# Kernel tuning notes

Measured on AMD Instinct MI355X. Metric: run time of the kernel, lower is better.

The kernel has to match this reference:

```python
import jax, jax.numpy as jnp
import numpy as np

N_NODES = 100000
N_EDGES = 1200000
NODE_IN = 64
EDGE_IN = 32
HIDDEN = 64


def _glorot(key, shape):
    fan_in, fan_out = shape[0], shape[1]
    s = jnp.sqrt(2.0 / (fan_in + fan_out))
    return jax.random.normal(key, shape, dtype=jnp.float32) * s


def setup_inputs() -> dict:
    key = jax.random.key(0)
    ks = jax.random.split(key, 16)
    inp = {
        "x": jax.random.normal(ks[0], (N_NODES, NODE_IN), dtype=jnp.float32),
        "edge_index": jax.random.randint(ks[1], (2, N_EDGES), 0, N_NODES, dtype=jnp.int64),
        "edge_attr": jax.random.normal(ks[2], (N_EDGES, EDGE_IN), dtype=jnp.float32),
        # SAGE layer 0 (in=NODE_IN -> HIDDEN): lin_l (neighbors, has bias), lin_r (root)
        "w_l0": _glorot(ks[3], (NODE_IN, HIDDEN)),
        "w_r0": _glorot(ks[4], (NODE_IN, HIDDEN)),
        "b0": jnp.zeros((HIDDEN,), jnp.float32),
        "ln_g0": jnp.ones((HIDDEN,), jnp.float32),
        "ln_b0": jnp.zeros((HIDDEN,), jnp.float32),
        # SAGE layer 1 (HIDDEN -> HIDDEN)
        "w_l1": _glorot(ks[5], (HIDDEN, HIDDEN)),
        "w_r1": _glorot(ks[6], (HIDDEN, HIDDEN)),
        "b1": jnp.zeros((HIDDEN,), jnp.float32),
        "ln_g1": jnp.ones((HIDDEN,), jnp.float32),
        "ln_b1": jnp.zeros((HIDDEN,), jnp.float32),
        # Edge classifier MLP: in_dim = 3*HIDDEN + EDGE_IN = 224
        "cw1": _glorot(ks[7], (3 * HIDDEN + EDGE_IN, HIDDEN)),
        "cb1": jnp.zeros((HIDDEN,), jnp.float32),
        "cw2": _glorot(ks[8], (HIDDEN, HIDDEN // 2)),
        "cb2": jnp.zeros((HIDDEN // 2,), jnp.float32),
        "cw3": _glorot(ks[9], (HIDDEN // 2, 1)),
        "cb3": jnp.zeros((1,), jnp.float32),
    }
    return inp


def _sage_conv(x, src, dst, w_l, w_r, b):
    # mean-aggregate source features at destination nodes (PyG SAGEConv, aggr='mean')
    n = x.shape[0]
    msg = x[src]  # [E, F] gather
    agg = jax.ops.segment_sum(msg, dst, num_segments=n)
    cnt = jax.ops.segment_sum(jnp.ones((src.shape[0], 1), x.dtype), dst, num_segments=n)
    mean = agg / jnp.maximum(cnt, 1.0)
    return mean @ w_l + x @ w_r + b


def _layer_norm(x, g, b, eps=1e-5):
    mu = jnp.mean(x, axis=-1, keepdims=True)
    var = jnp.var(x, axis=-1, keepdims=True)
    return (x - mu) * jax.lax.rsqrt(var + eps) * g + b


def reference(x, edge_index, edge_attr,
              w_l0, w_r0, b0, ln_g0, ln_b0,
              w_l1, w_r1, b1, ln_g1, ln_b1,
              cw1, cb1, cw2, cb2, cw3, cb3):
    src, dst = edge_index[0], edge_index[1]
    # Encoder (eval mode: dropout is identity)
    h = jax.nn.relu(_layer_norm(_sage_conv(x, src, dst, w_l0, w_r0, b0), ln_g0, ln_b0))
    z = jax.nn.relu(_layer_norm(_sage_conv(h, src, dst, w_l1, w_r1, b1), ln_g1, ln_b1))
    # Edge classifier: gather-concat-MLP
    z_src = z[src]
    z_dst = z[dst]
    edge_repr = jnp.concatenate([z_src, z_dst, z_src * z_dst, edge_attr], axis=-1)
    h1 = jax.nn.relu(edge_repr @ cw1 + cb1)
    h2 = jax.nn.relu(h1 @ cw2 + cb2)
    logits = (h2 @ cw3 + cb3).squeeze(-1)  # [E]
    return logits
```

## Files before the change

### kernel.cpp

```cpp
#include <hip/hip_runtime.h>
#include <hip/hip_bf16.h>

#define N_NODES 100000
#define N_EDGES 1200000

typedef __attribute__((ext_vector_type(8))) short bfrag;
typedef __attribute__((ext_vector_type(4))) float ffrag;

union FragU { uint4 v; uint32_t u[4]; bfrag f; };

__device__ __forceinline__ ushort bfbits(float a) {
  union { __hip_bfloat16 h; ushort u; } c; c.h = __float2bfloat16(a); return c.u;
}
__device__ __forceinline__ uint32_t pkbf(float a, float b) {
  union { __hip_bfloat162 h; uint32_t u; } c;
  c.h = __float22bfloat162_rn(float2{a, b}); return c.u;
}
__device__ __forceinline__ uint32_t mul2bf(uint32_t a, uint32_t b) {
  union { uint32_t u; __hip_bfloat162 h; } x, y, r;
  x.u = a; y.u = b; r.h = __hmul2(x.h, y.h); return r.u;
}
__device__ __forceinline__ float bflo(uint32_t u) { return __int_as_float(u << 16); }
__device__ __forceinline__ float bfhi(uint32_t u) { return __int_as_float(u & 0xffff0000u); }


__global__ void cvt_k(const float* __restrict__ x, ushort* __restrict__ xb, int n2) {
  int i = blockIdx.x * blockDim.x + threadIdx.x;
  if (i < n2) {
    float2 v = ((const float2*)x)[i];
    ((uint32_t*)xb)[i] = pkbf(v.x, v.y);
  }
}


__global__ void hist_k(const int* __restrict__ ei, int* __restrict__ deg,
                       int* __restrict__ rank, int E) {
  int e = blockIdx.x * blockDim.x + threadIdx.x;
  if (e < E) rank[e] = atomicAdd(&deg[ei[E + e]], 1);
}

__global__ __launch_bounds__(1024) void scan1_k(const int* __restrict__ deg,
                                                int* __restrict__ off,
                                                int* __restrict__ bsum, int n) {
  __shared__ int wpart[16];
  __shared__ int wpre[16];
  int tid = threadIdx.x, lane = tid & 63, wid = tid >> 6;
  int i = blockIdx.x * 1024 + tid;
  int v = (i < n) ? deg[i] : 0;
  int x = v;
  #pragma unroll
  for (int o = 1; o < 64; o <<= 1) {
    int y = __shfl_up(x, o);
    if (lane >= o) x += y;
  }
  if (lane == 63) wpart[wid] = x;
  __syncthreads();
  if (tid == 0) {
    int run = 0;
    #pragma unroll
    for (int w = 0; w < 16; w++) { int t = wpart[w]; wpre[w] = run; run += t; }
    bsum[blockIdx.x] = run;
  }
  __syncthreads();
  if (i < n) off[i] = x - v + wpre[wid];
}

__global__ void scan2_k(const int* __restrict__ bsum, int* __restrict__ bpre,
                        int* __restrict__ off, int nb, int n) {
  if (threadIdx.x == 0) {
    int run = 0;
    for (int b = 0; b < nb; b++) { int t = bsum[b]; bpre[b] = run; run += t; }
    off[n] = run;
  }
}

__global__ __launch_bounds__(1024) void scan3_k(int* __restrict__ off,
                                                const int* __restrict__ bpre, int n) {
  int i = blockIdx.x * 1024 + threadIdx.x;
  if (i < n) off[i] += bpre[blockIdx.x];
}

__global__ void fill_k(const int* __restrict__ ei, const int* __restrict__ off,
                       const int* __restrict__ rank, int* __restrict__ csr, int E) {
  int e = blockIdx.x * blockDim.x + threadIdx.x;
  if (e < E) {
    int d = ei[E + e];
    int p = off[d] + rank[e];
    __builtin_nontemporal_store(ei[e], &csr[p]);
  }
}


__global__ __launch_bounds__(256) void agg_k(
    const ushort* __restrict__ Xb, const int* __restrict__ off, const int* __restrict__ csr,
    ushort* __restrict__ aggout, int n) {
  int lane = threadIdx.x & 63;
  int quad = lane >> 4, f8 = lane & 15;
  int wave = blockIdx.x * 4 + (threadIdx.x >> 6);
  int nw = gridDim.x * 4;
  int nquads = (n + 3) >> 2;
  const uint2* X2 = (const uint2*)Xb;
  for (int p = wave; p < nquads; p += nw) {
    int i = p * 4 + quad;
    int ic = i < n ? i : n - 1;
    int s0 = off[ic], s1 = off[ic + 1];
    float a0 = 0.f, a1 = 0.f, a2 = 0.f, a3 = 0.f;
    for (int j = s0; j < s1; j += 8) {
      int id[8]; uint2 us[8];
      #pragma unroll
      for (int u = 0; u < 8; u++) {
        int jj = j + u;
        id[u] = csr[jj < s1 ? jj : s1 - 1];
      }
      #pragma unroll
      for (int u = 0; u < 8; u++) us[u] = X2[(size_t)id[u] * 16 + f8];
      #pragma unroll
      for (int u = 0; u < 8; u++) {
        if (j + u < s1) {
          a0 += bflo(us[u].x); a1 += bfhi(us[u].x);
          a2 += bflo(us[u].y); a3 += bfhi(us[u].y);
        }
      }
    }
    if (i < n) {
      float rdeg = 1.f / fmaxf((float)(s1 - s0), 1.f);
      uint2 w;
      w.x = pkbf(a0 * rdeg, a1 * rdeg);
      w.y = pkbf(a2 * rdeg, a3 * rdeg);
      ((uint2*)aggout)[(size_t)i * 16 + f8] = w;
    }
  }
}


__global__ __launch_bounds__(256) void node_k(
    const ushort* __restrict__ agg, const ushort* __restrict__ selfb,
    const float* __restrict__ wl, const float* __restrict__ wr,
    const float* __restrict__ bias, const float* __restrict__ g, const float* __restrict__ lb,
    ushort* __restrict__ outb, int n) {
  __shared__ ushort wt[64 * 128];
  const int tid = threadIdx.x;
  for (int i = tid; i < 8192; i += 256) {
    int k = i >> 6, nn = i & 63;
    float v = (k < 64) ? wl[k * 64 + nn] : wr[(k - 64) * 64 + nn];
    wt[nn * 128 + (((k >> 3) ^ (nn & 7)) * 8) + (k & 7)] = bfbits(v);
  }
  __syncthreads();
  const int lane = tid & 63, wid = tid >> 6;
  const int ln = lane & 15, q = lane >> 4;
  float bias_n[4], g_n[4], lb_n[4];
  #pragma unroll
  for (int nt = 0; nt < 4; nt++) {
    bias_n[nt] = bias[nt * 16 + ln];
    g_n[nt] = g[nt * 16 + ln];
    lb_n[nt] = lb[nt * 16 + ln];
  }
  const int ntiles = (n + 15) >> 4;
  for (int t = blockIdx.x * 4 + wid; t < ntiles; t += gridDim.x * 4) {
    int node = t * 16 + ln;
    int nc = node < n ? node : n - 1;
    FragU afr[4];
    #pragma unroll
    for (int kk = 0; kk < 2; kk++) {
      afr[kk].v     = ((const uint4*)agg)[(size_t)nc * 8 + kk * 4 + q];
      afr[2 + kk].v = ((const uint4*)selfb)[(size_t)nc * 8 + kk * 4 + q];
    }
    ffrag acc[4];
    #pragma unroll
    for (int nt = 0; nt < 4; nt++) acc[nt] = ffrag{0.f, 0.f, 0.f, 0.f};
    #pragma unroll
    for (int kk = 0; kk < 4; kk++) {
      bfrag a = afr[kk].f;
      #pragma unroll
      for (int nt = 0; nt < 4; nt++) {
        int nn = nt * 16 + ln;
        int b = kk * 4 + q;
        const bfrag* bp = (const bfrag*)&wt[nn * 128 + ((b ^ (nn & 7)) * 8)];
        acc[nt] = __builtin_amdgcn_mfma_f32_16x16x32_bf16(a, *bp, acc[nt], 0, 0, 0);
      }
    }
    #pragma unroll
    for (int r = 0; r < 4; r++) {
      int m = t * 16 + q * 4 + r;
      float o[4];
      #pragma unroll
      for (int nt = 0; nt < 4; nt++) o[nt] = acc[nt][r] + bias_n[nt];
      float s = (o[0] + o[1]) + (o[2] + o[3]);
      #pragma unroll
      for (int mm = 1; mm < 16; mm <<= 1) s += __shfl_xor(s, mm);
      float mu = s * (1.f / 64.f);
      float v2 = 0.f;
      #pragma unroll
      for (int nt = 0; nt < 4; nt++) { float d2 = o[nt] - mu; v2 += d2 * d2; }
      #pragma unroll
      for (int mm = 1; mm < 16; mm <<= 1) v2 += __shfl_xor(v2, mm);
      float rs = rsqrtf(v2 * (1.f / 64.f) + 1e-5f);
      if (m < n) {
        #pragma unroll
        for (int nt = 0; nt < 4; nt++) {
          float y = fmaxf((o[nt] - mu) * rs * g_n[nt] + lb_n[nt], 0.f);
          outb[(size_t)m * 64 + nt * 16 + ln] = bfbits(y);
        }
      }
    }
  }
}


__global__ __launch_bounds__(256) void edge_mfma_k(
    const int* __restrict__ ei, const float* __restrict__ ea,
    const ushort* __restrict__ zb,
    const float* __restrict__ cw1, const float* __restrict__ cb1,
    const float* __restrict__ cw2, const float* __restrict__ cb2,
    const float* __restrict__ cw3, const float* __restrict__ cb3,
    float* __restrict__ out, int E) {
  __shared__ ushort wt1[64 * 256];
  __shared__ ushort h1b[4][16 * 64];
  const int tid = threadIdx.x;

  for (int i = tid; i < 224 * 64; i += 256) {
    int k = i >> 6, n = i & 63;
    int blk = k >> 3;
    wt1[n * 256 + ((blk ^ (n & 7)) * 8) + (k & 7)] = bfbits(cw1[i]);
  }
  __syncthreads();

  const int lane = tid & 63, wid = tid >> 6;
  const int ln = lane & 15, q = lane >> 4;

  float cb1v[4];
  #pragma unroll
  for (int t = 0; t < 4; t++) cb1v[t] = cb1[t * 16 + ln];
  float cb2a = cb2[ln], cb2b = cb2[16 + ln];
  float w3a = cw3[ln], w3b = cw3[16 + ln];
  float cb3v = cb3[0];

  FragU w2f[2][2];
  #pragma unroll
  for (int t2 = 0; t2 < 2; t2++) {
    #pragma unroll
    for (int kk = 0; kk < 2; kk++) {
      #pragma unroll
      for (int p = 0; p < 4; p++) {
        int k = kk * 32 + q * 8 + p * 2;
        int n = t2 * 16 + ln;
        w2f[t2][kk].u[p] = pkbf(cw2[k * 32 + n], cw2[(k + 1) * 32 + n]);
      }
    }
  }

  ushort* hb = h1b[wid];
  const int ntiles = E >> 4;
  const int stride = gridDim.x * 4;
  int t = blockIdx.x * 4 + wid;

  FragU curz[4]; float4 ceal, ceah;
  if (t < ntiles) {
    int e = t * 16 + ln;
    int s = ei[e], d = ei[E + e];
    curz[0].v = ((const uint4*)zb)[(size_t)s * 8 + q];
    curz[1].v = ((const uint4*)zb)[(size_t)s * 8 + 4 + q];
    curz[2].v = ((const uint4*)zb)[(size_t)d * 8 + q];
    curz[3].v = ((const uint4*)zb)[(size_t)d * 8 + 4 + q];
    ceal = ((const float4*)ea)[(size_t)e * 8 + q * 2];
    ceah = ((const float4*)ea)[(size_t)e * 8 + q * 2 + 1];
  }

  for (; t < ntiles; t += stride) {
    int tn = t + stride;
    FragU nz[4]; float4 neal, neah;
    if (tn < ntiles) {
      int e2 = tn * 16 + ln;
      int s2 = ei[e2], d2 = ei[E + e2];
      nz[0].v = ((const uint4*)zb)[(size_t)s2 * 8 + q];
      nz[1].v = ((const uint4*)zb)[(size_t)s2 * 8 + 4 + q];
      nz[2].v = ((const uint4*)zb)[(size_t)d2 * 8 + q];
      nz[3].v = ((const uint4*)zb)[(size_t)d2 * 8 + 4 + q];
      neal = ((const float4*)ea)[(size_t)e2 * 8 + q * 2];
      neah = ((const float4*)ea)[(size_t)e2 * 8 + q * 2 + 1];
    }

    FragU afr[7];
    afr[0] = curz[0]; afr[1] = curz[1]; afr[2] = curz[2]; afr[3] = curz[3];
    #pragma unroll
    for (int kk = 0; kk < 2; kk++) {
      #pragma unroll
      for (int p = 0; p < 4; p++)
        afr[4 + kk].u[p] = mul2bf(curz[kk].u[p], curz[2 + kk].u[p]);
    }
    afr[6].u[0] = pkbf(ceal.x, ceal.y); afr[6].u[1] = pkbf(ceal.z, ceal.w);
    afr[6].u[2] = pkbf(ceah.x, ceah.y); afr[6].u[3] = pkbf(ceah.z, ceah.w);

    ffrag acc1[4];
    #pragma unroll
    for (int tt = 0; tt < 4; tt++) acc1[tt] = ffrag{0.f, 0.f, 0.f, 0.f};
    #pragma unroll
    for (int kk = 0; kk < 7; kk++) {
      bfrag a = afr[kk].f;
      #pragma unroll
      for (int tt = 0; tt < 4; tt++) {
        int n = tt * 16 + ln;
        int b = kk * 4 + q;
        const bfrag* bp = (const bfrag*)&wt1[n * 256 + ((b ^ (n & 7)) * 8)];
        acc1[tt] = __builtin_amdgcn_mfma_f32_16x16x32_bf16(a, *bp, acc1[tt], 0, 0, 0);
      }
    }

    #pragma unroll
    for (int tt = 0; tt < 4; tt++) {
      #pragma unroll
      for (int r = 0; r < 4; r++) {
        int m = q * 4 + r;
        int col = tt * 16 + ln;
        float v = fmaxf(acc1[tt][r] + cb1v[tt], 0.f);
        hb[m * 64 + (((col >> 3) ^ (m & 7)) * 8) + (col & 7)] = bfbits(v);
      }
    }

    ffrag acc2[2];
    acc2[0] = ffrag{0.f, 0.f, 0.f, 0.f};
    acc2[1] = ffrag{0.f, 0.f, 0.f, 0.f};
    #pragma unroll
    for (int kk = 0; kk < 2; kk++) {
      int b = kk * 4 + q;
      const bfrag* ap = (const bfrag*)&hb[ln * 64 + ((b ^ (ln & 7)) * 8)];
      bfrag a2 = *ap;
      acc2[0] = __builtin_amdgcn_mfma_f32_16x16x32_bf16(a2, w2f[0][kk].f, acc2[0], 0, 0, 0);
      acc2[1] = __builtin_amdgcn_mfma_f32_16x16x32_bf16(a2, w2f[1][kk].f, acc2[1], 0, 0, 0);
    }

    float p0, p1, p2, p3;
    {
      p0 = fmaxf(acc2[0][0] + cb2a, 0.f) * w3a + fmaxf(acc2[1][0] + cb2b, 0.f) * w3b;
      p1 = fmaxf(acc2[0][1] + cb2a, 0.f) * w3a + fmaxf(acc2[1][1] + cb2b, 0.f) * w3b;
      p2 = fmaxf(acc2[0][2] + cb2a, 0.f) * w3a + fmaxf(acc2[1][2] + cb2b, 0.f) * w3b;
      p3 = fmaxf(acc2[0][3] + cb2a, 0.f) * w3a + fmaxf(acc2[1][3] + cb2b, 0.f) * w3b;
    }
    #pragma unroll
    for (int o = 1; o < 16; o <<= 1) {
      p0 += __shfl_xor(p0, o);
      p1 += __shfl_xor(p1, o);
      p2 += __shfl_xor(p2, o);
      p3 += __shfl_xor(p3, o);
    }
    float keep = (ln == 0) ? p0 : (ln == 1) ? p1 : (ln == 2) ? p2 : p3;
    if (ln < 4) out[t * 16 + q * 4 + ln] = keep + cb3v;

    curz[0] = nz[0]; curz[1] = nz[1]; curz[2] = nz[2]; curz[3] = nz[3];
    ceal = neal; ceah = neah;
  }
}


extern "C" void kernel_launch(void* const* d_in, const int* in_sizes, int n_in,
                              void* d_out, int out_size, void* d_ws, size_t ws_size,
                              hipStream_t stream) {
  const float* x   = (const float*)d_in[0];
  const int*   ei  = (const int*)d_in[1];
  const float* ea  = (const float*)d_in[2];
  const float* wl0 = (const float*)d_in[3];
  const float* wr0 = (const float*)d_in[4];
  const float* b0  = (const float*)d_in[5];
  const float* g0  = (const float*)d_in[6];
  const float* lb0 = (const float*)d_in[7];
  const float* wl1 = (const float*)d_in[8];
  const float* wr1 = (const float*)d_in[9];
  const float* b1  = (const float*)d_in[10];
  const float* g1  = (const float*)d_in[11];
  const float* lb1 = (const float*)d_in[12];
  const float* cw1 = (const float*)d_in[13];
  const float* cb1 = (const float*)d_in[14];
  const float* cw2 = (const float*)d_in[15];
  const float* cb2 = (const float*)d_in[16];
  const float* cw3 = (const float*)d_in[17];
  const float* cb3 = (const float*)d_in[18];
  float* out = (float*)d_out;
  const int N = N_NODES, E = N_EDGES;
  const int NB = (N + 1023) / 1024;

  uintptr_t pp = (uintptr_t)d_ws;
  auto alloc = [&](size_t bytes) {
    uintptr_t r = (pp + 255) & ~(uintptr_t)255; pp = r + bytes; return (void*)r;
  };
  int* deg  = (int*)alloc((size_t)N * 4);
  int* off  = (int*)alloc((size_t)(N + 1) * 4);
  int* rank = (int*)alloc((size_t)E * 4);
  int* csr  = (int*)alloc((size_t)E * 4);
  int* bsum = (int*)alloc((size_t)NB * 4);
  int* bpre = (int*)alloc((size_t)NB * 4);
  ushort* xb  = (ushort*)alloc((size_t)N * 64 * 2);
  ushort* agg = (ushort*)alloc((size_t)N * 64 * 2);
  ushort* hb  = (ushort*)alloc((size_t)N * 64 * 2);
  ushort* zb  = (ushort*)alloc((size_t)N * 64 * 2);

  hipMemsetAsync(deg, 0, (size_t)N * 4, stream);
  cvt_k<<<(N * 32 + 255) / 256, 256, 0, stream>>>(x, xb, N * 32);
  hist_k<<<(E + 255) / 256, 256, 0, stream>>>(ei, deg, rank, E);
  scan1_k<<<NB, 1024, 0, stream>>>(deg, off, bsum, N);
  scan2_k<<<1, 64, 0, stream>>>(bsum, bpre, off, NB, N);
  scan3_k<<<NB, 1024, 0, stream>>>(off, bpre, N);
  fill_k<<<(E + 255) / 256, 256, 0, stream>>>(ei, off, rank, csr, E);
  agg_k<<<2048, 256, 0, stream>>>(xb, off, csr, agg, N);
  node_k<<<512, 256, 0, stream>>>(agg, xb, wl0, wr0, b0, g0, lb0, hb, N);
  agg_k<<<2048, 256, 0, stream>>>(hb, off, csr, agg, N);
  node_k<<<512, 256, 0, stream>>>(agg, hb, wl1, wr1, b1, g1, lb1, zb, N);
  edge_mfma_k<<<1024, 256, 0, stream>>>(ei, ea, zb, cw1, cb1, cw2, cb2, cw3, cb3, out, E);
}
```

Measured before the change: 515.1 us.

## Widen aggregation loads to 16B per lane and transpose edge MLP MFMA

The aggregation kernel now gives each node 8 lanes that each load 16 bytes, instead of 16 lanes loading 8 bytes, and launches more blocks so every node gets its own wave slot. The edge kernel swaps the MFMA operand roles: weights become the A operand and edge features the B operand. The first-layer bias is folded in as an extra K row of ones, and h1 is written to LDS as packed 8-byte stores instead of scalar 2-byte stores. Launch bounds now request 4 waves per SIMD, which trades register budget for occupancy and adds one padded MFMA K-step per tile.

```diff
diff --git a/kernel.cpp b/kernel.cpp
--- a/kernel.cpp
+++ b/kernel.cpp
@@ -95,39 +95,42 @@
     const ushort* __restrict__ Xb, const int* __restrict__ off, const int* __restrict__ csr,
     ushort* __restrict__ aggout, int n) {
   int lane = threadIdx.x & 63;
-  int quad = lane >> 4, f8 = lane & 15;
+  int oct = lane >> 3, f4 = lane & 7;
   int wave = blockIdx.x * 4 + (threadIdx.x >> 6);
   int nw = gridDim.x * 4;
-  int nquads = (n + 3) >> 2;
-  const uint2* X2 = (const uint2*)Xb;
-  for (int p = wave; p < nquads; p += nw) {
-    int i = p * 4 + quad;
+  const uint4* X4 = (const uint4*)Xb;
+  for (int i = wave * 8 + oct; i < n + 7; i += nw * 8) {
     int ic = i < n ? i : n - 1;
     int s0 = off[ic], s1 = off[ic + 1];
     float a0 = 0.f, a1 = 0.f, a2 = 0.f, a3 = 0.f;
+    float a4 = 0.f, a5 = 0.f, a6 = 0.f, a7 = 0.f;
     for (int j = s0; j < s1; j += 8) {
-      int id[8]; uint2 us[8];
+      int id[8]; uint4 us[8];
       #pragma unroll
       for (int u = 0; u < 8; u++) {
         int jj = j + u;
         id[u] = csr[jj < s1 ? jj : s1 - 1];
       }
       #pragma unroll
-      for (int u = 0; u < 8; u++) us[u] = X2[(size_t)id[u] * 16 + f8];
+      for (int u = 0; u < 8; u++) us[u] = X4[(size_t)id[u] * 8 + f4];
       #pragma unroll
       for (int u = 0; u < 8; u++) {
         if (j + u < s1) {
           a0 += bflo(us[u].x); a1 += bfhi(us[u].x);
           a2 += bflo(us[u].y); a3 += bfhi(us[u].y);
+          a4 += bflo(us[u].z); a5 += bfhi(us[u].z);
+          a6 += bflo(us[u].w); a7 += bfhi(us[u].w);
         }
       }
     }
     if (i < n) {
       float rdeg = 1.f / fmaxf((float)(s1 - s0), 1.f);
-      uint2 w;
+      uint4 w;
       w.x = pkbf(a0 * rdeg, a1 * rdeg);
       w.y = pkbf(a2 * rdeg, a3 * rdeg);
-      ((uint2*)aggout)[(size_t)i * 16 + f8] = w;
+      w.z = pkbf(a4 * rdeg, a5 * rdeg);
+      w.w = pkbf(a6 * rdeg, a7 * rdeg);
+      ((uint4*)aggout)[(size_t)i * 8 + f4] = w;
     }
   }
 }
@@ -207,7 +210,7 @@
 }
 
 
-__global__ __launch_bounds__(256) void edge_mfma_k(
+__global__ __launch_bounds__(256, 4) void edge_mfma_k(
     const int* __restrict__ ei, const float* __restrict__ ea,
     const ushort* __restrict__ zb,
     const float* __restrict__ cw1, const float* __restrict__ cb1,
@@ -218,19 +221,16 @@
   __shared__ ushort h1b[4][16 * 64];
   const int tid = threadIdx.x;
 
-  for (int i = tid; i < 224 * 64; i += 256) {
-    int k = i >> 6, n = i & 63;
-    int blk = k >> 3;
-    wt1[n * 256 + ((blk ^ (n & 7)) * 8) + (k & 7)] = bfbits(cw1[i]);
+  for (int i = tid; i < 64 * 256; i += 256) {
+    int n = i >> 8, k = i & 255;
+    float v = (k < 224) ? cw1[k * 64 + n] : (k == 224 ? cb1[n] : 0.f);
+    wt1[n * 256 + (((k >> 3) ^ (n & 7)) * 8) + (k & 7)] = bfbits(v);
   }
   __syncthreads();
 
   const int lane = tid & 63, wid = tid >> 6;
   const int ln = lane & 15, q = lane >> 4;
 
-  float cb1v[4];
-  #pragma unroll
-  for (int t = 0; t < 4; t++) cb1v[t] = cb1[t * 16 + ln];
   float cb2a = cb2[ln], cb2b = cb2[16 + ln];
   float w3a = cw3[ln], w3b = cw3[16 + ln];
   float cb3v = cb3[0];
@@ -249,6 +249,7 @@
     }
   }
 
+  const uint32_t a7lo = (q == 0) ? 0x00003F80u : 0u;
   ushort* hb = h1b[wid];
   const int ntiles = E >> 4;
   const int stride = gridDim.x * 4;
@@ -280,7 +281,7 @@
       neah = ((const float4*)ea)[(size_t)e2 * 8 + q * 2 + 1];
     }
 
-    FragU afr[7];
+    FragU afr[8];
     afr[0] = curz[0]; afr[1] = curz[1]; afr[2] = curz[2]; afr[3] = curz[3];
     #pragma unroll
     for (int kk = 0; kk < 2; kk++) {
@@ -290,31 +291,29 @@
     }
     afr[6].u[0] = pkbf(ceal.x, ceal.y); afr[6].u[1] = pkbf(ceal.z, ceal.w);
     afr[6].u[2] = pkbf(ceah.x, ceah.y); afr[6].u[3] = pkbf(ceah.z, ceah.w);
+    afr[7].u[0] = a7lo; afr[7].u[1] = 0; afr[7].u[2] = 0; afr[7].u[3] = 0;
 
     ffrag acc1[4];
     #pragma unroll
-    for (int tt = 0; tt < 4; tt++) acc1[tt] = ffrag{0.f, 0.f, 0.f, 0.f};
-    #pragma unroll
-    for (int kk = 0; kk < 7; kk++) {
-      bfrag a = afr[kk].f;
-      #pragma unroll
-      for (int tt = 0; tt < 4; tt++) {
-        int n = tt * 16 + ln;
-        int b = kk * 4 + q;
-        const bfrag* bp = (const bfrag*)&wt1[n * 256 + ((b ^ (n & 7)) * 8)];
-        acc1[tt] = __builtin_amdgcn_mfma_f32_16x16x32_bf16(a, *bp, acc1[tt], 0, 0, 0);
-      }
-    }
-
-    #pragma unroll
-    for (int tt = 0; tt < 4; tt++) {
-      #pragma unroll
-      for (int r = 0; r < 4; r++) {
-        int m = q * 4 + r;
-        int col = tt * 16 + ln;
-        float v = fmaxf(acc1[tt][r] + cb1v[tt], 0.f);
-        hb[m * 64 + (((col >> 3) ^ (m & 7)) * 8) + (col & 7)] = bfbits(v);
-      }
+    for (int mt = 0; mt < 4; mt++) acc1[mt] = ffrag{0.f, 0.f, 0.f, 0.f};
+    #pragma unroll
+    for (int kk = 0; kk < 8; kk++) {
+      bfrag b = afr[kk].f;
+      #pragma unroll
+      for (int mt = 0; mt < 4; mt++) {
+        int m = mt * 16 + ln;
+        const bfrag* ap = (const bfrag*)&wt1[m * 256 + (((kk * 4 + q) ^ (ln & 7)) * 8)];
+        acc1[mt] = __builtin_amdgcn_mfma_f32_16x16x32_bf16(*ap, b, acc1[mt], 0, 0, 0);
+      }
+    }
+
+    #pragma unroll
+    for (int mt = 0; mt < 4; mt++) {
+      float v0 = fmaxf(acc1[mt][0], 0.f), v1 = fmaxf(acc1[mt][1], 0.f);
+      float v2 = fmaxf(acc1[mt][2], 0.f), v3 = fmaxf(acc1[mt][3], 0.f);
+      uint2 w; w.x = pkbf(v0, v1); w.y = pkbf(v2, v3);
+      int blk = (mt * 2 + (q >> 1)) ^ (ln & 7);
+      *(uint2*)&hb[ln * 64 + blk * 8 + (q & 1) * 4] = w;
     }
 
     ffrag acc2[2];
@@ -322,8 +321,7 @@
     acc2[1] = ffrag{0.f, 0.f, 0.f, 0.f};
     #pragma unroll
     for (int kk = 0; kk < 2; kk++) {
-      int b = kk * 4 + q;
-      const bfrag* ap = (const bfrag*)&hb[ln * 64 + ((b ^ (ln & 7)) * 8)];
+      const bfrag* ap = (const bfrag*)&hb[ln * 64 + (((kk * 4 + q) ^ (ln & 7)) * 8)];
       bfrag a2 = *ap;
       acc2[0] = __builtin_amdgcn_mfma_f32_16x16x32_bf16(a2, w2f[0][kk].f, acc2[0], 0, 0, 0);
       acc2[1] = __builtin_amdgcn_mfma_f32_16x16x32_bf16(a2, w2f[1][kk].f, acc2[1], 0, 0, 0);
@@ -400,9 +398,9 @@
   scan2_k<<<1, 64, 0, stream>>>(bsum, bpre, off, NB, N);
   scan3_k<<<NB, 1024, 0, stream>>>(off, bpre, N);
   fill_k<<<(E + 255) / 256, 256, 0, stream>>>(ei, off, rank, csr, E);
-  agg_k<<<2048, 256, 0, stream>>>(xb, off, csr, agg, N);
+  agg_k<<<3136, 256, 0, stream>>>(xb, off, csr, agg, N);
   node_k<<<512, 256, 0, stream>>>(agg, xb, wl0, wr0, b0, g0, lb0, hb, N);
-  agg_k<<<2048, 256, 0, stream>>>(hb, off, csr, agg, N);
+  agg_k<<<3136, 256, 0, stream>>>(hb, off, csr, agg, N);
   node_k<<<512, 256, 0, stream>>>(agg, hb, wl1, wr1, b1, g1, lb1, zb, N);
   edge_mfma_k<<<1024, 256, 0, stream>>>(ei, ea, zb, cw1, cb1, cw2, cb2, cw3, cb3, out, E);
 }
```

After: 801.3 us. 55.6% more time.
